# Kernel tuning notes

Hardware: AMD Instinct MI355X
Metric: run time of the kernel (lower is better)

The kernel has to match this reference:

```python
import jax, jax.numpy as jnp
import numpy as np

L, N, E, D, H = 3, 20000, 320000, 128, 4
EPS = 1.1920929e-07  # torch RMSNorm default eps = finfo(float32).eps
NEG_SLOPE = 0.2      # PyG GATConv leaky_relu negative_slope


def rmsnorm(x, w):
    return x * jax.lax.rsqrt(jnp.mean(x * x, axis=-1, keepdims=True) + EPS) * w


def setup_inputs() -> dict:
    key = jax.random.key(0)
    ks = jax.random.split(key, 13)
    s = 0.02
    x = jax.random.normal(ks[0], (N, D), jnp.float32)
    src = jax.random.randint(ks[1], (E,), 0, N, dtype=jnp.int64)
    dst = jax.random.randint(ks[2], (E,), 0, N, dtype=jnp.int64)
    dst = jnp.where(dst == src, (dst + 1) % N, dst)  # no pre-existing self loops
    edge_index = jnp.stack([src, dst])
    return {
        "x": x,
        "W_gat": jax.random.normal(ks[3], (L, D, H * D), jnp.float32) * s,
        "att_src": jax.random.normal(ks[4], (L, H, D), jnp.float32) * s,
        "att_dst": jax.random.normal(ks[5], (L, H, D), jnp.float32) * s,
        "bias_gat": jax.random.normal(ks[6], (L, D), jnp.float32) * s,
        "W1": jax.random.normal(ks[7], (L, D, D), jnp.float32) * s,
        "b1": jax.random.normal(ks[8], (L, D), jnp.float32) * s,
        "W2": jax.random.normal(ks[9], (L, D, D), jnp.float32) * s,
        "b2": jax.random.normal(ks[10], (L, D), jnp.float32) * s,
        "norm1_w": jnp.ones((L, D), jnp.float32),
        "norm2_w": jnp.ones((L, D), jnp.float32),
        "edge_index": edge_index,
    }


def reference(x, W_gat, att_src, att_dst, bias_gat, W1, b1, W2, b2, norm1_w, norm2_w, edge_index):
    # PyG GATConv adds self loops by default
    loops = jnp.arange(N, dtype=edge_index.dtype)
    src = jnp.concatenate([edge_index[0], loops])  # [E+N]
    dst = jnp.concatenate([edge_index[1], loops])
    for i in range(L):
        # --- GATConv(hidden, hidden, heads=H, concat=False), dropout=0 (eval) ---
        xp = (x @ W_gat[i]).reshape(N, H, D)               # [N,H,D]
        a_s = jnp.einsum('nhd,hd->nh', xp, att_src[i])     # [N,H]
        a_d = jnp.einsum('nhd,hd->nh', xp, att_dst[i])
        e = jax.nn.leaky_relu(a_s[src] + a_d[dst], NEG_SLOPE)  # [E+N,H]
        m = jax.ops.segment_max(e, dst, num_segments=N)
        ex = jnp.exp(e - m[dst])
        denom = jax.ops.segment_sum(ex, dst, num_segments=N)
        alpha = ex / denom[dst]                             # segment softmax over incoming edges
        agg = jax.ops.segment_sum(alpha[:, :, None] * xp[src], dst, num_segments=N)  # [N,H,D]
        x_att = agg.mean(axis=1) + bias_gat[i]              # concat=False -> head mean, then bias
        # --- residual + RMSNorm ---
        x = rmsnorm(x + x_att, norm1_w[i])
        # --- FFN ---
        h = jax.nn.relu(x @ W1[i] + b1[i])
        h = h @ W2[i] + b2[i]
        x = rmsnorm(x + h, norm2_w[i])
    return x
```

## Files before the change

kernel.cpp:

```cpp
#include <hip/hip_runtime.h>
#include <hip/hip_bf16.h>

#define N_NODES 20000
#define NEDGE   320000
#define DIM     128
#define NH      4
#define HD      512
#define LAYERS  3
#define EPS_RMS 1.1920929e-07f
#define SLOPE   0.2f
#define NTILES  (N_NODES >> 4)

typedef __bf16 bf16_t;
typedef __bf16 bf16v2 __attribute__((ext_vector_type(2)));
typedef __bf16 bf16v8 __attribute__((ext_vector_type(8)));
typedef float  f32v4  __attribute__((ext_vector_type(4)));
typedef float  f32v2  __attribute__((ext_vector_type(2)));

__device__ __forceinline__ int clamp_node(int s) {
    return ((unsigned)s >= (unsigned)N_NODES) ? 0 : s;
}
__device__ __forceinline__ float leaky(float e) { return e > 0.f ? e : SLOPE * e; }
__device__ __forceinline__ unsigned char enc_fp8(float v) {
    int p = __builtin_amdgcn_cvt_pk_fp8_f32(v, v, 0, false);
    return (unsigned char)(p & 0xff);
}
__device__ __forceinline__ unsigned short enc_fp8_pair(float a, float b) {
    int p = __builtin_amdgcn_cvt_pk_fp8_f32(a, b, 0, false);
    return (unsigned short)(p & 0xffff);
}

__device__ __forceinline__ bool wave_detect_bf16(const unsigned short* xh) {
    int lane = threadIdx.x & 63;
    unsigned short hw = xh[2 * lane];
    int e = (hw >> 7) & 0xff;
    unsigned long long b = __ballot(e >= 96 && e <= 140);
    return __popcll(b) >= 48;
}
__device__ __forceinline__ bool wave_detect_i64(const int* ei) {
    int lane = threadIdx.x & 63;
    unsigned long long b = __ballot(ei[2 * lane + 1] != 0);
    return b == 0ULL;
}
__device__ __forceinline__ float raw_elem(const void* in, size_t j, bool isbf) {
    return isbf ? (float)((const bf16_t*)in)[j] : ((const float*)in)[j];
}
__device__ __forceinline__ bf16_t cvt_elem(const void* in, size_t j, bool isbf) {
    return isbf ? ((const bf16_t*)in)[j] : (bf16_t)((const float*)in)[j];
}
__device__ __forceinline__ int edge_src(const int* ei, int e, bool is64) {
    return clamp_node(is64 ? ei[2 * e] : ei[e]);
}
__device__ __forceinline__ int edge_dst(const int* ei, int e, bool is64) {
    return clamp_node(is64 ? ei[2 * NEDGE + 2 * e] : ei[NEDGE + e]);
}

__global__ __launch_bounds__(256) void prep_v(const void* x, const void* Wg,
                                              const void* aS, const void* aD,
                                              float* __restrict__ vS, float* __restrict__ vD,
                                              int* __restrict__ deg) {
    int gid = blockIdx.x * 256 + threadIdx.x;
    for (int i = gid; i < N_NODES; i += gridDim.x * 256) deg[i] = 0;
    bool isbf = wave_detect_bf16((const unsigned short*)x);
    int w = gid >> 6;
    if (w >= LAYERS * DIM * NH * 2) return;
    int lane = threadIdx.x & 63;
    int sd = w & 1, h = (w >> 1) & 3, k = (w >> 3) & 127, l = w >> 10;
    const void* att = sd ? aD : aS;
    size_t wbase = (size_t)l * DIM * HD + (size_t)k * HD + h * DIM;
    size_t abase = (size_t)l * NH * DIM + (size_t)h * DIM;
    int c = 2 * lane;
    float p = raw_elem(Wg, wbase + c, isbf) * raw_elem(att, abase + c, isbf)
            + raw_elem(Wg, wbase + c + 1, isbf) * raw_elem(att, abase + c + 1, isbf);
#pragma unroll
    for (int msk = 1; msk < 64; msk <<= 1) p += __shfl_xor(p, msk);
    if (lane == 0) {
        float* dst = sd ? vD : vS;
        dst[l * HD + h * DIM + k] = p;
    }
}

__global__ __launch_bounds__(256) void mega_setup(
        const void* x, const void* Wg, const void* W1, const void* W2,
        const void* bg, const void* b1, const void* b2, const void* n1, const void* n2,
        bf16_t* xb, bf16_t* WmixP, bf16_t* W1P, bf16_t* W2P,
        bf16_t* bgc, bf16_t* b1c, bf16_t* b2c, bf16_t* n1c, bf16_t* n2c,
        const int* ei, int* deg,
        const float* vS, const float* vD,
        float* a_s, float* a_d, unsigned short* x8,
        int convBlocks, int histBlocks) {
    const int NX  = N_NODES * DIM;
    const int NWG = LAYERS * DIM * HD;
    const int NW1 = LAYERS * DIM * DIM;
    const int NV  = LAYERS * DIM;
    int b = (int)blockIdx.x;
    if (b >= convBlocks + histBlocks) {
        bool isbf = wave_detect_bf16((const unsigned short*)x);
        int lane = threadIdx.x & 63;
        int n = (b - convBlocks - histBlocks) * 4 + (int)(threadIdx.x >> 6);
        if (n >= N_NODES) return;
        int c = 2 * lane;
        float f0 = raw_elem(x, (size_t)n * DIM + c, isbf);
        float f1 = raw_elem(x, (size_t)n * DIM + c + 1, isbf);
        x8[n * 64 + lane] = enc_fp8_pair(f0, f1);
#pragma unroll
        for (int h = 0; h < NH; ++h) {
            float ps = f0 * vS[h * DIM + c] + f1 * vS[h * DIM + c + 1];
            float pd = f0 * vD[h * DIM + c] + f1 * vD[h * DIM + c + 1];
#pragma unroll
            for (int msk = 1; msk < 64; msk <<= 1) {
                ps += __shfl_xor(ps, msk);
                pd += __shfl_xor(pd, msk);
            }
            if (lane == 0) {
                a_s[n * 4 + h] = ps;
                a_d[n * 4 + h] = pd;
            }
        }
        return;
    }
    if (b >= convBlocks) {
        bool is64 = wave_detect_i64(ei);
        int e = (b - convBlocks) * 256 + threadIdx.x;
        if (e < NEDGE) atomicAdd(&deg[edge_dst(ei, e, is64)], 1);
        return;
    }
    bool isbf = wave_detect_bf16((const unsigned short*)x);
    int i = b * 256 + threadIdx.x;
    if (i < NX) { xb[i] = cvt_elem(x, i, isbf); return; }
    i -= NX;
    if (i < NWG) {
        int l = i >> 16;
        int r = i & 65535;
        int j = r & 7;
        int lane2 = (r >> 3) & 63;
        int mm = lane2 & 15, kqq = lane2 >> 4;
        int tt = (r >> 9) & 1;
        int kk = (r >> 10) & 15;
        int wvv = r >> 14;
        int kidx = kk * 32 + kqq * 8 + j;
        int h = kidx >> 7, kp = kidx & 127;
        int c = 32 * wvv + tt * 16 + mm;
        WmixP[i] = cvt_elem(Wg, (size_t)l * DIM * HD + (size_t)kp * HD + h * DIM + c, isbf);
        return;
    }
    i -= NWG;
    if (i < NW1) {
        int l = i / 16384;
        int r = i & 16383;
        int j = r & 7;
        int lane2 = (r >> 3) & 63;
        int mm = lane2 & 15, kqq = lane2 >> 4;
        int tt = (r >> 9) & 1;
        int ks = (r >> 10) & 3;
        int wvv = r >> 12;
        int k = ks * 32 + kqq * 8 + j;
        int c = 32 * wvv + tt * 16 + mm;
        W1P[i] = cvt_elem(W1, (size_t)l * DIM * DIM + (size_t)k * DIM + c, isbf);
        return;
    }
    i -= NW1;
    if (i < NW1) {
        int l = i / 16384;
        int r = i & 16383;
        int j = r & 7;
        int lane2 = (r >> 3) & 63;
        int mm = lane2 & 15, kqq = lane2 >> 4;
        int tt = (r >> 9) & 1;
        int ks = (r >> 10) & 3;
        int wvv = r >> 12;
        int k = ks * 32 + kqq * 8 + j;
        int c = 32 * wvv + tt * 16 + mm;
        W2P[i] = cvt_elem(W2, (size_t)l * DIM * DIM + (size_t)k * DIM + c, isbf);
        return;
    }
    i -= NW1;
    if (i >= 5 * NV) return;
    int seg = i / NV, k = i - seg * NV;
    if (seg == 0) bgc[k] = cvt_elem(bg, k, isbf);
    else if (seg == 1) b1c[k] = cvt_elem(b1, k, isbf);
    else if (seg == 2) b2c[k] = cvt_elem(b2, k, isbf);
    else if (seg == 3) n1c[k] = cvt_elem(n1, k, isbf);
    else n2c[k] = cvt_elem(n2, k, isbf);
}

__global__ __launch_bounds__(1024) void scan_kernel(const int* __restrict__ deg,
                                                    int* __restrict__ row_ptr,
                                                    int* __restrict__ cursor) {
    __shared__ int wsum[16];
    int tid = threadIdx.x, lane = tid & 63, wv = tid >> 6;
    int v[20];
    int base = tid * 20;
    int tot = 0;
    if (base < N_NODES) {
        const int4* d4 = reinterpret_cast<const int4*>(deg + base);
#pragma unroll
        for (int j = 0; j < 5; ++j) {
            int4 q = d4[j];
            v[4 * j]     = q.x;
            v[4 * j + 1] = q.y;
            v[4 * j + 2] = q.z;
            v[4 * j + 3] = q.w;
        }
#pragma unroll
        for (int i = 0; i < 20; ++i) tot += v[i];
    }
    int x = tot;
#pragma unroll
    for (int off = 1; off < 64; off <<= 1) {
        int t = __shfl_up(x, off);
        if (lane >= off) x += t;
    }
    if (lane == 63) wsum[wv] = x;
    __syncthreads();
    if (wv == 0) {
        int s = (lane < 16) ? wsum[lane] : 0;
#pragma unroll
        for (int off = 1; off < 16; off <<= 1) {
            int t = __shfl_up(s, off);
            if (lane >= off) s += t;
        }
        if (lane < 16) wsum[lane] = s;
    }
    __syncthreads();
    int off0 = ((wv == 0) ? 0 : wsum[wv - 1]) + (x - tot);
    if (tid == 0) row_ptr[0] = 0;
    if (base < N_NODES) {
        int run = off0;
#pragma unroll
        for (int i = 0; i < 20; ++i) {
            run += v[i];
            row_ptr[base + i + 1] = run;
            cursor[base + i] = run - v[i];
        }
    }
}

__global__ void fill_kernel(const int* __restrict__ ei, int* __restrict__ cursor,
                            int* __restrict__ csr_src) {
    bool is64 = wave_detect_i64(ei);
    int e = blockIdx.x * blockDim.x + threadIdx.x;
    if (e < NEDGE) {
        int d = edge_dst(ei, e, is64);
        int pos = atomicAdd(&cursor[d], 1);
        if ((unsigned)pos < (unsigned)NEDGE) csr_src[pos] = edge_src(ei, e, is64);
    }
}

__global__ __launch_bounds__(256) void gat_gather(const int* __restrict__ row_ptr,
                                                  const int* __restrict__ csr_src,
                                                  const float* __restrict__ a_s,
                                                  const float* __restrict__ a_d,
                                                  const unsigned short* __restrict__ x8,
                                                  bf16_t* __restrict__ y) {
    __shared__ float4 wsh[4][64];
    __shared__ int    ssh[4][64];
    int n = (int)((blockIdx.x * blockDim.x + threadIdx.x) >> 6);
    if (n >= N_NODES) return;
    int wv = (int)(threadIdx.x >> 6) & 3;
    int lane = threadIdx.x & 63;
    int beg = row_ptr[n];
    int deg = row_ptr[n + 1] - beg;
    if (deg < 0) deg = 0;
    if (deg > NEDGE) deg = NEDGE;
    if (beg < 0) beg = 0;
    if (beg > NEDGE - deg) beg = NEDGE - deg;

    const float4* a_s4 = reinterpret_cast<const float4*>(a_s);
    const float4 adv = reinterpret_cast<const float4*>(a_d)[n];
    const float4 avs = a_s4[n];
    unsigned short pself = x8[n * 64 + lane];
    float4 wself = {__expf(leaky(avs.x + adv.x)), __expf(leaky(avs.y + adv.y)),
                    __expf(leaky(avs.z + adv.z)), __expf(leaky(avs.w + adv.w))};

    float acc[8];
    {
        f32v2 f = __builtin_amdgcn_cvt_pk_f32_fp8((int)pself, false);
        acc[0] = wself.x * f[0]; acc[1] = wself.x * f[1];
        acc[2] = wself.y * f[0]; acc[3] = wself.y * f[1];
        acc[4] = wself.z * f[0]; acc[5] = wself.z * f[1];
        acc[6] = wself.w * f[0]; acc[7] = wself.w * f[1];
    }

    float4 zl = {0.f, 0.f, 0.f, 0.f};
    for (int c0 = 0; c0 < deg; c0 += 64) {
        int cnt = deg - c0; if (cnt > 64) cnt = 64;
        if (lane < cnt) {
            int s = clamp_node(csr_src[beg + c0 + lane]);
            float4 av = a_s4[s];
            float4 w = {__expf(leaky(av.x + adv.x)), __expf(leaky(av.y + adv.y)),
                        __expf(leaky(av.z + adv.z)), __expf(leaky(av.w + adv.w))};
            zl.x += w.x; zl.y += w.y; zl.z += w.z; zl.w += w.w;
            wsh[wv][lane] = w;
            ssh[wv][lane] = s << 6;
        }
        for (int u0 = 0; u0 < cnt; u0 += 8) {
            int uc = cnt - u0; if (uc > 8) uc = 8;
            unsigned short xe[8]; float4 w[8];
#pragma unroll
            for (int u = 0; u < 8; ++u) {
                if (u < uc) {
                    int sb = ssh[wv][u0 + u];
                    w[u] = wsh[wv][u0 + u];
                    xe[u] = x8[sb + lane];
                }
            }
#pragma unroll
            for (int u = 0; u < 8; ++u) {
                if (u < uc) {
                    f32v2 f = __builtin_amdgcn_cvt_pk_f32_fp8((int)xe[u], false);
                    acc[0] += w[u].x * f[0]; acc[1] += w[u].x * f[1];
                    acc[2] += w[u].y * f[0]; acc[3] += w[u].y * f[1];
                    acc[4] += w[u].z * f[0]; acc[5] += w[u].z * f[1];
                    acc[6] += w[u].w * f[0]; acc[7] += w[u].w * f[1];
                }
            }
        }
    }
    float4 zr = zl;
#pragma unroll
    for (int msk = 1; msk < 64; msk <<= 1) {
        zr.x += __shfl_xor(zr.x, msk);
        zr.y += __shfl_xor(zr.y, msk);
        zr.z += __shfl_xor(zr.z, msk);
        zr.w += __shfl_xor(zr.w, msk);
    }
    float4 z4 = {wself.x + zr.x, wself.y + zr.y, wself.z + zr.z, wself.w + zr.w};
    float4 ih4 = {1.f / z4.x, 1.f / z4.y, 1.f / z4.z, 1.f / z4.w};
    int c = 2 * lane;
#pragma unroll
    for (int h = 0; h < NH; ++h) {
        float ih = h == 0 ? ih4.x : h == 1 ? ih4.y : h == 2 ? ih4.z : ih4.w;
        bf16v2 o;
        o[0] = (bf16_t)(acc[h * 2 + 0] * ih);
        o[1] = (bf16_t)(acc[h * 2 + 1] * ih);
        *reinterpret_cast<bf16v2*>(&y[(size_t)n * HD + h * DIM + c]) = o;
    }
}

template <int MODE>
__global__ __launch_bounds__(256) void mix_ffn(
        const bf16_t* __restrict__ y,
        const bf16_t* __restrict__ WmixP, const bf16_t* __restrict__ bg,
        const bf16_t* __restrict__ n1w, const bf16_t* __restrict__ xb,
        const bf16_t* __restrict__ W1P, const bf16_t* __restrict__ b1,
        const bf16_t* __restrict__ W2P, const bf16_t* __restrict__ b2,
        const bf16_t* __restrict__ n2w, void* __restrict__ out,
        const float* __restrict__ vS, const float* __restrict__ vD,
        float* __restrict__ a_s_n, float* __restrict__ a_d_n,
        unsigned char* __restrict__ x8_n) {
    __shared__ bf16_t ylds[16][524];
    __shared__ bf16_t xm[16][140];
    __shared__ float  ssq_p[16][4];
    __shared__ float  asd_p[4][16][8];
    bf16_t (*hh)[140] = reinterpret_cast<bf16_t (*)[140]>(&ylds[0][0]);

    int tile = blockIdx.x;
    int wv = threadIdx.x >> 6;
    int lane = threadIdx.x & 63;
    int m = lane & 15, kq = lane >> 4;

    const bf16_t* ybase = y + (size_t)tile * 16 * HD;
#pragma unroll
    for (int it = 0; it < 8; ++it) {
        int f = it * 2048 + (int)threadIdx.x * 8;
        int row = f >> 9, col = f & 511;
        *reinterpret_cast<bf16v8*>(&ylds[row][col]) =
            *reinterpret_cast<const bf16v8*>(ybase + f);
    }
    __syncthreads();

    f32v4 accm[2];
    accm[0] = (f32v4){0.f, 0.f, 0.f, 0.f};
    accm[1] = (f32v4){0.f, 0.f, 0.f, 0.f};
#pragma unroll
    for (int kk = 0; kk < 16; ++kk) {
        bf16v8 a = *reinterpret_cast<const bf16v8*>(&ylds[m][kk * 32 + kq * 8]);
#pragma unroll
        for (int tt = 0; tt < 2; ++tt) {
            bf16v8 b = *reinterpret_cast<const bf16v8*>(
                WmixP + ((((wv * 16 + kk) * 2 + tt) << 9) + lane * 8));
            accm[tt] = __builtin_amdgcn_mfma_f32_16x16x32_bf16(a, b, accm[tt], 0, 0, 0);
        }
    }
    float vals[2][4];
    {
        float sp[4] = {0.f, 0.f, 0.f, 0.f};
#pragma unroll
        for (int tt = 0; tt < 2; ++tt) {
            int col = 32 * wv + tt * 16 + m;
            float bv = (float)bg[col];
#pragma unroll
            for (int r = 0; r < 4; ++r) {
                int gr = tile * 16 + kq * 4 + r;
                float v = 0.25f * accm[tt][r] + bv + (float)xb[(size_t)gr * DIM + col];
                vals[tt][r] = v;
                sp[r] += v * v;
            }
        }
#pragma unroll
        for (int r = 0; r < 4; ++r) {
            sp[r] += __shfl_xor(sp[r], 1); sp[r] += __shfl_xor(sp[r], 2);
            sp[r] += __shfl_xor(sp[r], 4); sp[r] += __shfl_xor(sp[r], 8);
            if (m == r) ssq_p[kq * 4 + r][wv] = sp[r];
        }
    }
    __syncthreads();
    {
#pragma unroll
        for (int r = 0; r < 4; ++r) {
            int row = kq * 4 + r;
            float s = ssq_p[row][0] + ssq_p[row][1] + ssq_p[row][2] + ssq_p[row][3];
            float scale = rsqrtf(s * (1.f / 128.f) + EPS_RMS);
#pragma unroll
            for (int tt = 0; tt < 2; ++tt) {
                int col = 32 * wv + tt * 16 + m;
                xm[row][col] = (bf16_t)(vals[tt][r] * scale * (float)n1w[col]);
            }
        }
    }
    __syncthreads();

    f32v4 acc1[2];
    acc1[0] = (f32v4){0.f, 0.f, 0.f, 0.f};
    acc1[1] = (f32v4){0.f, 0.f, 0.f, 0.f};
#pragma unroll
    for (int ks = 0; ks < 4; ++ks) {
        bf16v8 a = *reinterpret_cast<const bf16v8*>(&xm[m][ks * 32 + kq * 8]);
#pragma unroll
        for (int tt = 0; tt < 2; ++tt) {
            bf16v8 b = *reinterpret_cast<const bf16v8*>(
                W1P + ((((wv * 4 + ks) * 2 + tt) << 9) + lane * 8));
            acc1[tt] = __builtin_amdgcn_mfma_f32_16x16x32_bf16(a, b, acc1[tt], 0, 0, 0);
        }
    }
#pragma unroll
    for (int tt = 0; tt < 2; ++tt) {
        int col = 32 * wv + tt * 16 + m;
        float bv = (float)b1[col];
#pragma unroll
        for (int r = 0; r < 4; ++r) {
            float v = acc1[tt][r] + bv;
            hh[kq * 4 + r][col] = (bf16_t)(v > 0.f ? v : 0.f);
        }
    }
    __syncthreads();
    f32v4 acc2[2];
    acc2[0] = (f32v4){0.f, 0.f, 0.f, 0.f};
    acc2[1] = (f32v4){0.f, 0.f, 0.f, 0.f};
#pragma unroll
    for (int ks = 0; ks < 4; ++ks) {
        bf16v8 a = *reinterpret_cast<const bf16v8*>(&hh[m][ks * 32 + kq * 8]);
#pragma unroll
        for (int tt = 0; tt < 2; ++tt) {
            bf16v8 b = *reinterpret_cast<const bf16v8*>(
                W2P + ((((wv * 4 + ks) * 2 + tt) << 9) + lane * 8));
            acc2[tt] = __builtin_amdgcn_mfma_f32_16x16x32_bf16(a, b, acc2[tt], 0, 0, 0);
        }
    }
    float vals2[2][4];
    {
        float sp[4] = {0.f, 0.f, 0.f, 0.f};
#pragma unroll
        for (int tt = 0; tt < 2; ++tt) {
            int col = 32 * wv + tt * 16 + m;
            float bv = (float)b2[col];
#pragma unroll
            for (int r = 0; r < 4; ++r) {
                float v = acc2[tt][r] + bv + (float)xm[kq * 4 + r][col];
                vals2[tt][r] = v;
                sp[r] += v * v;
            }
        }
#pragma unroll
        for (int r = 0; r < 4; ++r) {
            sp[r] += __shfl_xor(sp[r], 1); sp[r] += __shfl_xor(sp[r], 2);
            sp[r] += __shfl_xor(sp[r], 4); sp[r] += __shfl_xor(sp[r], 8);
            if (m == r) ssq_p[kq * 4 + r][wv] = sp[r];
        }
    }
    __syncthreads();
    float o2[2][4];
#pragma unroll
    for (int r = 0; r < 4; ++r) {
        int row = kq * 4 + r;
        int gr = tile * 16 + row;
        float s = ssq_p[row][0] + ssq_p[row][1] + ssq_p[row][2] + ssq_p[row][3];
        float scale = rsqrtf(s * (1.f / 128.f) + EPS_RMS);
#pragma unroll
        for (int tt = 0; tt < 2; ++tt) {
            int col = 32 * wv + tt * 16 + m;
            float o = vals2[tt][r] * scale * (float)n2w[col];
            o2[tt][r] = o;
            if (MODE == 1) ((float*)out)[(size_t)gr * DIM + col] = o;
            else {
                ((bf16_t*)out)[(size_t)gr * DIM + col] = (bf16_t)o;
                x8_n[(size_t)gr * DIM + col] = enc_fp8(o);
            }
        }
    }
    if (MODE == 0) {
        float vs0[NH], vs1[NH], vd0[NH], vd1[NH];
        int col0 = 32 * wv + m, col1 = col0 + 16;
#pragma unroll
        for (int h = 0; h < NH; ++h) {
            vs0[h] = vS[h * DIM + col0]; vs1[h] = vS[h * DIM + col1];
            vd0[h] = vD[h * DIM + col0]; vd1[h] = vD[h * DIM + col1];
        }
#pragma unroll
        for (int r = 0; r < 4; ++r) {
#pragma unroll
            for (int h = 0; h < NH; ++h) {
                float ps = o2[0][r] * vs0[h] + o2[1][r] * vs1[h];
                float pd = o2[0][r] * vd0[h] + o2[1][r] * vd1[h];
                ps += __shfl_xor(ps, 1); ps += __shfl_xor(ps, 2);
                ps += __shfl_xor(ps, 4); ps += __shfl_xor(ps, 8);
                pd += __shfl_xor(pd, 1); pd += __shfl_xor(pd, 2);
                pd += __shfl_xor(pd, 4); pd += __shfl_xor(pd, 8);
                if (m == r * 4 + h) {
                    asd_p[wv][kq * 4 + r][h * 2 + 0] = ps;
                    asd_p[wv][kq * 4 + r][h * 2 + 1] = pd;
                }
            }
        }
        __syncthreads();
        int t = threadIdx.x;
        if (t < 128) {
            int row = t >> 3, idx = t & 7;
            float s = asd_p[0][row][idx] + asd_p[1][row][idx]
                    + asd_p[2][row][idx] + asd_p[3][row][idx];
            int gr = tile * 16 + row;
            if (idx & 1) a_d_n[gr * 4 + (idx >> 1)] = s;
            else         a_s_n[gr * 4 + (idx >> 1)] = s;
        }
    }
}

extern "C" void kernel_launch(void* const* d_in, const int* in_sizes, int n_in,
                              void* d_out, int out_size, void* d_ws, size_t ws_size,
                              hipStream_t stream) {
    const void* x_in   = d_in[0];
    const void* W_gat  = d_in[1];
    const void* att_s  = d_in[2];
    const void* att_d  = d_in[3];
    const void* bias_g = d_in[4];
    const void* W1     = d_in[5];
    const void* b1     = d_in[6];
    const void* W2     = d_in[7];
    const void* b2     = d_in[8];
    const void* n1w    = d_in[9];
    const void* n2w    = d_in[10];
    const int*  ei     = (const int*)d_in[11];

    char* ws = (char*)d_ws;
    size_t off = 0;
    auto alloc = [&](size_t bytes) {
        void* p = ws + off;
        off = (off + bytes + 255) & ~(size_t)255;
        return p;
    };
    bf16_t* WmixP   = (bf16_t*)alloc((size_t)LAYERS * HD * DIM * 2);
    bf16_t* W1P     = (bf16_t*)alloc((size_t)LAYERS * DIM * DIM * 2);
    bf16_t* W2P     = (bf16_t*)alloc((size_t)LAYERS * DIM * DIM * 2);
    bf16_t* xb      = (bf16_t*)alloc((size_t)N_NODES * DIM * 2);
    bf16_t* y       = (bf16_t*)alloc((size_t)N_NODES * HD * 2);
    unsigned short* x8a = (unsigned short*)alloc((size_t)N_NODES * DIM);
    unsigned short* x8b = (unsigned short*)alloc((size_t)N_NODES * DIM);
    float*  vS      = (float*)alloc((size_t)LAYERS * HD * 4);
    float*  vD      = (float*)alloc((size_t)LAYERS * HD * 4);
    float*  a_sA    = (float*)alloc((size_t)N_NODES * NH * 4);
    float*  a_dA    = (float*)alloc((size_t)N_NODES * NH * 4);
    float*  a_sB    = (float*)alloc((size_t)N_NODES * NH * 4);
    float*  a_dB    = (float*)alloc((size_t)N_NODES * NH * 4);
    int*    deg     = (int*)alloc((size_t)N_NODES * 4);
    int*    cursor  = (int*)alloc((size_t)N_NODES * 4);
    int*    row_ptr = (int*)alloc((size_t)(N_NODES + 1) * 4);
    int*    csr     = (int*)alloc((size_t)NEDGE * 4);
    bf16_t* bgc     = (bf16_t*)alloc((size_t)LAYERS * DIM * 2);
    bf16_t* b1c     = (bf16_t*)alloc((size_t)LAYERS * DIM * 2);
    bf16_t* b2c     = (bf16_t*)alloc((size_t)LAYERS * DIM * 2);
    bf16_t* n1c     = (bf16_t*)alloc((size_t)LAYERS * DIM * 2);
    bf16_t* n2c     = (bf16_t*)alloc((size_t)LAYERS * DIM * 2);

    prep_v<<<(LAYERS * DIM * NH * 2 * 64 + 255) / 256, 256, 0, stream>>>(
        x_in, W_gat, att_s, att_d, vS, vD, deg);

    const int NTOT = N_NODES * DIM + LAYERS * DIM * HD + 2 * LAYERS * DIM * DIM
                   + 5 * LAYERS * DIM;
    const int convBlocks = (NTOT + 255) / 256;
    const int histBlocks = (NEDGE + 255) / 256;
    const int asdBlocks  = (N_NODES + 3) / 4;
    mega_setup<<<convBlocks + histBlocks + asdBlocks, 256, 0, stream>>>(
        x_in, W_gat, W1, W2, bias_g, b1, b2, n1w, n2w,
        xb, WmixP, W1P, W2P, bgc, b1c, b2c, n1c, n2c,
        ei, deg, vS, vD, a_sA, a_dA, x8a, convBlocks, histBlocks);

    scan_kernel<<<1, 1024, 0, stream>>>(deg, row_ptr, cursor);
    fill_kernel<<<(NEDGE + 255) / 256, 256, 0, stream>>>(ei, cursor, csr);

    unsigned short* x8cur[2] = {x8a, x8b};
    float* asCur[2] = {a_sA, a_sB};
    float* adCur[2] = {a_dA, a_dB};
    for (int l = 0; l < LAYERS; ++l) {
        int ci = l & 1, ni = (l + 1) & 1;
        gat_gather<<<(N_NODES * 64 + 255) / 256, 256, 0, stream>>>(
            row_ptr, csr, asCur[ci], adCur[ci], x8cur[ci], y);
        if (l < LAYERS - 1) {
            mix_ffn<0><<<NTILES, 256, 0, stream>>>(
                y, WmixP + (size_t)l * HD * DIM, bgc + (size_t)l * DIM,
                n1c + (size_t)l * DIM, xb,
                W1P + (size_t)l * DIM * DIM, b1c + (size_t)l * DIM,
                W2P + (size_t)l * DIM * DIM, b2c + (size_t)l * DIM,
                n2c + (size_t)l * DIM, xb,
                vS + (size_t)(l + 1) * HD, vD + (size_t)(l + 1) * HD,
                asCur[ni], adCur[ni], (unsigned char*)x8cur[ni]);
        } else {
            mix_ffn<1><<<NTILES, 256, 0, stream>>>(
                y, WmixP + (size_t)l * HD * DIM, bgc + (size_t)l * DIM,
                n1c + (size_t)l * DIM, xb,
                W1P + (size_t)l * DIM * DIM, b1c + (size_t)l * DIM,
                W2P + (size_t)l * DIM * DIM, b2c + (size_t)l * DIM,
                n2c + (size_t)l * DIM, d_out,
                nullptr, nullptr, nullptr, nullptr, nullptr);
        }
    }
}
```

Measured before the change: 313.3 us.

## Fuse whole pipeline into one persistent cooperative kernel with grid syncs

Replaces the sequence of setup, scan, fill, gather and mix/FFN launches with a single cooperative persistent kernel. Phases are separated by grid-wide barriers and use grid-stride loops sized from occupancy queries. The aim is to remove launch gaps and tail effects across roughly ten kernels. The cost is grid-sync overhead, a block count capped at 1024, and a single-block scan phase that may serialize. A fallback to the multi-kernel path is kept.

```diff
diff --git a/kernel.cpp b/kernel.cpp
--- a/kernel.cpp
+++ b/kernel.cpp
@@ -1,5 +1,8 @@
 #include <hip/hip_runtime.h>
 #include <hip/hip_bf16.h>
+#include <hip/hip_cooperative_groups.h>
+
+namespace cg = cooperative_groups;
 
 #define N_NODES 20000
 #define NEDGE   320000
@@ -11,6 +14,13 @@
 #define SLOPE   0.2f
 #define NTILES  (N_NODES >> 4)
 
+#define NWGC  (LAYERS * DIM * HD)
+#define NW1C  (LAYERS * DIM * DIM)
+#define NVC   (LAYERS * DIM)
+#define NPACK (NWGC + 2 * NW1C + 5 * NVC)
+
+#define SMEM_BYTES 23552
+
 typedef __bf16 bf16_t;
 typedef __bf16 bf16v2 __attribute__((ext_vector_type(2)));
 typedef __bf16 bf16v8 __attribute__((ext_vector_type(8)));
@@ -54,6 +64,529 @@
 __device__ __forceinline__ int edge_dst(const int* ei, int e, bool is64) {
     return clamp_node(is64 ? ei[2 * NEDGE + 2 * e] : ei[NEDGE + e]);
 }
+
+
+__device__ __forceinline__ void pack_item(int i, bool isbf,
+        const void* Wg, const void* W1, const void* W2,
+        const void* bg, const void* b1, const void* b2,
+        const void* n1, const void* n2,
+        bf16_t* WmixP, bf16_t* W1P, bf16_t* W2P,
+        bf16_t* bgc, bf16_t* b1c, bf16_t* b2c, bf16_t* n1c, bf16_t* n2c) {
+    if (i < NWGC) {
+        int l = i >> 16;
+        int r = i & 65535;
+        int j = r & 7;
+        int lane2 = (r >> 3) & 63;
+        int mm = lane2 & 15, kqq = lane2 >> 4;
+        int tt = (r >> 9) & 1;
+        int kk = (r >> 10) & 15;
+        int wvv = r >> 14;
+        int kidx = kk * 32 + kqq * 8 + j;
+        int h = kidx >> 7, kp = kidx & 127;
+        int c = 32 * wvv + tt * 16 + mm;
+        WmixP[i] = cvt_elem(Wg, (size_t)l * DIM * HD + (size_t)kp * HD + h * DIM + c, isbf);
+        return;
+    }
+    i -= NWGC;
+    if (i < NW1C) {
+        int l = i / 16384;
+        int r = i & 16383;
+        int j = r & 7;
+        int lane2 = (r >> 3) & 63;
+        int mm = lane2 & 15, kqq = lane2 >> 4;
+        int tt = (r >> 9) & 1;
+        int ks = (r >> 10) & 3;
+        int wvv = r >> 12;
+        int k = ks * 32 + kqq * 8 + j;
+        int c = 32 * wvv + tt * 16 + mm;
+        W1P[i] = cvt_elem(W1, (size_t)l * DIM * DIM + (size_t)k * DIM + c, isbf);
+        return;
+    }
+    i -= NW1C;
+    if (i < NW1C) {
+        int l = i / 16384;
+        int r = i & 16383;
+        int j = r & 7;
+        int lane2 = (r >> 3) & 63;
+        int mm = lane2 & 15, kqq = lane2 >> 4;
+        int tt = (r >> 9) & 1;
+        int ks = (r >> 10) & 3;
+        int wvv = r >> 12;
+        int k = ks * 32 + kqq * 8 + j;
+        int c = 32 * wvv + tt * 16 + mm;
+        W2P[i] = cvt_elem(W2, (size_t)l * DIM * DIM + (size_t)k * DIM + c, isbf);
+        return;
+    }
+    i -= NW1C;
+    if (i >= 5 * NVC) return;
+    int seg = i / NVC, k = i - seg * NVC;
+    if (seg == 0) bgc[k] = cvt_elem(bg, k, isbf);
+    else if (seg == 1) b1c[k] = cvt_elem(b1, k, isbf);
+    else if (seg == 2) b2c[k] = cvt_elem(b2, k, isbf);
+    else if (seg == 3) n1c[k] = cvt_elem(n1, k, isbf);
+    else n2c[k] = cvt_elem(n2, k, isbf);
+}
+
+__device__ __forceinline__ void asd_node(int n, int lane, bool isbf, const void* x,
+        const float* __restrict__ vS, const float* __restrict__ vD,
+        float* __restrict__ a_s, float* __restrict__ a_d,
+        unsigned short* __restrict__ x8) {
+    int c = 2 * lane;
+    float f0 = raw_elem(x, (size_t)n * DIM + c, isbf);
+    float f1 = raw_elem(x, (size_t)n * DIM + c + 1, isbf);
+    x8[n * 64 + lane] = enc_fp8_pair(f0, f1);
+#pragma unroll
+    for (int h = 0; h < NH; ++h) {
+        float ps = f0 * vS[h * DIM + c] + f1 * vS[h * DIM + c + 1];
+        float pd = f0 * vD[h * DIM + c] + f1 * vD[h * DIM + c + 1];
+#pragma unroll
+        for (int msk = 1; msk < 64; msk <<= 1) {
+            ps += __shfl_xor(ps, msk);
+            pd += __shfl_xor(pd, msk);
+        }
+        if (lane == 0) {
+            a_s[n * 4 + h] = ps;
+            a_d[n * 4 + h] = pd;
+        }
+    }
+}
+
+__device__ __forceinline__ void gather_node(int n, int lane,
+        float4* wshw, int* sshw,
+        const int* __restrict__ row_ptr, const int* __restrict__ csr_src,
+        const float* __restrict__ a_s, const float* __restrict__ a_d,
+        const unsigned short* __restrict__ x8, bf16_t* __restrict__ y) {
+    int beg = row_ptr[n];
+    int deg = row_ptr[n + 1] - beg;
+    if (deg < 0) deg = 0;
+    if (deg > NEDGE) deg = NEDGE;
+    if (beg < 0) beg = 0;
+    if (beg > NEDGE - deg) beg = NEDGE - deg;
+
+    const float4* a_s4 = reinterpret_cast<const float4*>(a_s);
+    const float4 adv = reinterpret_cast<const float4*>(a_d)[n];
+    const float4 avs = a_s4[n];
+    unsigned short pself = x8[n * 64 + lane];
+    float4 wself = {__expf(leaky(avs.x + adv.x)), __expf(leaky(avs.y + adv.y)),
+                    __expf(leaky(avs.z + adv.z)), __expf(leaky(avs.w + adv.w))};
+
+    float acc[8];
+    {
+        f32v2 f = __builtin_amdgcn_cvt_pk_f32_fp8((int)pself, false);
+        acc[0] = wself.x * f[0]; acc[1] = wself.x * f[1];
+        acc[2] = wself.y * f[0]; acc[3] = wself.y * f[1];
+        acc[4] = wself.z * f[0]; acc[5] = wself.z * f[1];
+        acc[6] = wself.w * f[0]; acc[7] = wself.w * f[1];
+    }
+
+    float4 zl = {0.f, 0.f, 0.f, 0.f};
+    for (int c0 = 0; c0 < deg; c0 += 64) {
+        int cnt = deg - c0; if (cnt > 64) cnt = 64;
+        if (lane < cnt) {
+            int s = clamp_node(csr_src[beg + c0 + lane]);
+            float4 av = a_s4[s];
+            float4 w = {__expf(leaky(av.x + adv.x)), __expf(leaky(av.y + adv.y)),
+                        __expf(leaky(av.z + adv.z)), __expf(leaky(av.w + adv.w))};
+            zl.x += w.x; zl.y += w.y; zl.z += w.z; zl.w += w.w;
+            wshw[lane] = w;
+            sshw[lane] = s << 6;
+        }
+        for (int u0 = 0; u0 < cnt; u0 += 8) {
+            int uc = cnt - u0; if (uc > 8) uc = 8;
+            unsigned short xe[8]; float4 w[8];
+#pragma unroll
+            for (int u = 0; u < 8; ++u) {
+                if (u < uc) {
+                    int sb = sshw[u0 + u];
+                    w[u] = wshw[u0 + u];
+                    xe[u] = x8[sb + lane];
+                }
+            }
+#pragma unroll
+            for (int u = 0; u < 8; ++u) {
+                if (u < uc) {
+                    f32v2 f = __builtin_amdgcn_cvt_pk_f32_fp8((int)xe[u], false);
+                    acc[0] += w[u].x * f[0]; acc[1] += w[u].x * f[1];
+                    acc[2] += w[u].y * f[0]; acc[3] += w[u].y * f[1];
+                    acc[4] += w[u].z * f[0]; acc[5] += w[u].z * f[1];
+                    acc[6] += w[u].w * f[0]; acc[7] += w[u].w * f[1];
+                }
+            }
+        }
+    }
+    float4 zr = zl;
+#pragma unroll
+    for (int msk = 1; msk < 64; msk <<= 1) {
+        zr.x += __shfl_xor(zr.x, msk);
+        zr.y += __shfl_xor(zr.y, msk);
+        zr.z += __shfl_xor(zr.z, msk);
+        zr.w += __shfl_xor(zr.w, msk);
+    }
+    float4 z4 = {wself.x + zr.x, wself.y + zr.y, wself.z + zr.z, wself.w + zr.w};
+    float4 ih4 = {1.f / z4.x, 1.f / z4.y, 1.f / z4.z, 1.f / z4.w};
+    int c = 2 * lane;
+#pragma unroll
+    for (int h = 0; h < NH; ++h) {
+        float ih = h == 0 ? ih4.x : h == 1 ? ih4.y : h == 2 ? ih4.z : ih4.w;
+        bf16v2 o;
+        o[0] = (bf16_t)(acc[h * 2 + 0] * ih);
+        o[1] = (bf16_t)(acc[h * 2 + 1] * ih);
+        *reinterpret_cast<bf16v2*>(&y[(size_t)n * HD + h * DIM + c]) = o;
+    }
+}
+
+__device__ __forceinline__ void mix_tile(char* smem, int tile, bool last,
+        const bf16_t* __restrict__ y,
+        const bf16_t* __restrict__ WmixP, const bf16_t* __restrict__ bg,
+        const bf16_t* __restrict__ n1w, const bf16_t* xb,
+        const bf16_t* __restrict__ W1P, const bf16_t* __restrict__ b1,
+        const bf16_t* __restrict__ W2P, const bf16_t* __restrict__ b2,
+        const bf16_t* __restrict__ n2w, void* out,
+        const float* __restrict__ vS, const float* __restrict__ vD,
+        float* __restrict__ a_s_n, float* __restrict__ a_d_n,
+        unsigned char* __restrict__ x8_n) {
+    bf16_t (*ylds)[524]    = reinterpret_cast<bf16_t(*)[524]>(smem);
+    bf16_t (*xm)[140]      = reinterpret_cast<bf16_t(*)[140]>(smem + 16768);
+    float  (*ssq_p)[4]     = reinterpret_cast<float(*)[4]>(smem + 21248);
+    float  (*asd_p)[16][8] = reinterpret_cast<float(*)[16][8]>(smem + 21504);
+    bf16_t (*hh)[140]      = reinterpret_cast<bf16_t(*)[140]>(smem);
+
+    int wv = (int)threadIdx.x >> 6;
+    int lane = (int)threadIdx.x & 63;
+    int m = lane & 15, kq = lane >> 4;
+
+    const bf16_t* ybase = y + (size_t)tile * 16 * HD;
+#pragma unroll
+    for (int it = 0; it < 8; ++it) {
+        int f = it * 2048 + (int)threadIdx.x * 8;
+        int row = f >> 9, col = f & 511;
+        *reinterpret_cast<bf16v8*>(&ylds[row][col]) =
+            *reinterpret_cast<const bf16v8*>(ybase + f);
+    }
+    __syncthreads();
+
+    f32v4 accm[2];
+    accm[0] = (f32v4){0.f, 0.f, 0.f, 0.f};
+    accm[1] = (f32v4){0.f, 0.f, 0.f, 0.f};
+#pragma unroll
+    for (int kk = 0; kk < 16; ++kk) {
+        bf16v8 a = *reinterpret_cast<const bf16v8*>(&ylds[m][kk * 32 + kq * 8]);
+#pragma unroll
+        for (int tt = 0; tt < 2; ++tt) {
+            bf16v8 b = *reinterpret_cast<const bf16v8*>(
+                WmixP + ((((wv * 16 + kk) * 2 + tt) << 9) + lane * 8));
+            accm[tt] = __builtin_amdgcn_mfma_f32_16x16x32_bf16(a, b, accm[tt], 0, 0, 0);
+        }
+    }
+    float vals[2][4];
+    {
+        float sp[4] = {0.f, 0.f, 0.f, 0.f};
+#pragma unroll
+        for (int tt = 0; tt < 2; ++tt) {
+            int col = 32 * wv + tt * 16 + m;
+            float bv = (float)bg[col];
+#pragma unroll
+            for (int r = 0; r < 4; ++r) {
+                int gr = tile * 16 + kq * 4 + r;
+                float v = 0.25f * accm[tt][r] + bv + (float)xb[(size_t)gr * DIM + col];
+                vals[tt][r] = v;
+                sp[r] += v * v;
+            }
+        }
+#pragma unroll
+        for (int r = 0; r < 4; ++r) {
+            sp[r] += __shfl_xor(sp[r], 1); sp[r] += __shfl_xor(sp[r], 2);
+            sp[r] += __shfl_xor(sp[r], 4); sp[r] += __shfl_xor(sp[r], 8);
+            if (m == r) ssq_p[kq * 4 + r][wv] = sp[r];
+        }
+    }
+    __syncthreads();
+    {
+#pragma unroll
+        for (int r = 0; r < 4; ++r) {
+            int row = kq * 4 + r;
+            float s = ssq_p[row][0] + ssq_p[row][1] + ssq_p[row][2] + ssq_p[row][3];
+            float scale = rsqrtf(s * (1.f / 128.f) + EPS_RMS);
+#pragma unroll
+            for (int tt = 0; tt < 2; ++tt) {
+                int col = 32 * wv + tt * 16 + m;
+                xm[row][col] = (bf16_t)(vals[tt][r] * scale * (float)n1w[col]);
+            }
+        }
+    }
+    __syncthreads();
+
+    f32v4 acc1[2];
+    acc1[0] = (f32v4){0.f, 0.f, 0.f, 0.f};
+    acc1[1] = (f32v4){0.f, 0.f, 0.f, 0.f};
+#pragma unroll
+    for (int ks = 0; ks < 4; ++ks) {
+        bf16v8 a = *reinterpret_cast<const bf16v8*>(&xm[m][ks * 32 + kq * 8]);
+#pragma unroll
+        for (int tt = 0; tt < 2; ++tt) {
+            bf16v8 b = *reinterpret_cast<const bf16v8*>(
+                W1P + ((((wv * 4 + ks) * 2 + tt) << 9) + lane * 8));
+            acc1[tt] = __builtin_amdgcn_mfma_f32_16x16x32_bf16(a, b, acc1[tt], 0, 0, 0);
+        }
+    }
+#pragma unroll
+    for (int tt = 0; tt < 2; ++tt) {
+        int col = 32 * wv + tt * 16 + m;
+        float bv = (float)b1[col];
+#pragma unroll
+        for (int r = 0; r < 4; ++r) {
+            float v = acc1[tt][r] + bv;
+            hh[kq * 4 + r][col] = (bf16_t)(v > 0.f ? v : 0.f);
+        }
+    }
+    __syncthreads();
+    f32v4 acc2[2];
+    acc2[0] = (f32v4){0.f, 0.f, 0.f, 0.f};
+    acc2[1] = (f32v4){0.f, 0.f, 0.f, 0.f};
+#pragma unroll
+    for (int ks = 0; ks < 4; ++ks) {
+        bf16v8 a = *reinterpret_cast<const bf16v8*>(&hh[m][ks * 32 + kq * 8]);
+#pragma unroll
+        for (int tt = 0; tt < 2; ++tt) {
+            bf16v8 b = *reinterpret_cast<const bf16v8*>(
+                W2P + ((((wv * 4 + ks) * 2 + tt) << 9) + lane * 8));
+            acc2[tt] = __builtin_amdgcn_mfma_f32_16x16x32_bf16(a, b, acc2[tt], 0, 0, 0);
+        }
+    }
+    float vals2[2][4];
+    {
+        float sp[4] = {0.f, 0.f, 0.f, 0.f};
+#pragma unroll
+        for (int tt = 0; tt < 2; ++tt) {
+            int col = 32 * wv + tt * 16 + m;
+            float bv = (float)b2[col];
+#pragma unroll
+            for (int r = 0; r < 4; ++r) {
+                float v = acc2[tt][r] + bv + (float)xm[kq * 4 + r][col];
+                vals2[tt][r] = v;
+                sp[r] += v * v;
+            }
+        }
+#pragma unroll
+        for (int r = 0; r < 4; ++r) {
+            sp[r] += __shfl_xor(sp[r], 1); sp[r] += __shfl_xor(sp[r], 2);
+            sp[r] += __shfl_xor(sp[r], 4); sp[r] += __shfl_xor(sp[r], 8);
+            if (m == r) ssq_p[kq * 4 + r][wv] = sp[r];
+        }
+    }
+    __syncthreads();
+    float o2[2][4];
+#pragma unroll
+    for (int r = 0; r < 4; ++r) {
+        int row = kq * 4 + r;
+        int gr = tile * 16 + row;
+        float s = ssq_p[row][0] + ssq_p[row][1] + ssq_p[row][2] + ssq_p[row][3];
+        float scale = rsqrtf(s * (1.f / 128.f) + EPS_RMS);
+#pragma unroll
+        for (int tt = 0; tt < 2; ++tt) {
+            int col = 32 * wv + tt * 16 + m;
+            float o = vals2[tt][r] * scale * (float)n2w[col];
+            o2[tt][r] = o;
+            if (last) ((float*)out)[(size_t)gr * DIM + col] = o;
+            else {
+                ((bf16_t*)out)[(size_t)gr * DIM + col] = (bf16_t)o;
+                x8_n[(size_t)gr * DIM + col] = enc_fp8(o);
+            }
+        }
+    }
+    if (!last) {
+        float vs0[NH], vs1[NH], vd0[NH], vd1[NH];
+        int col0 = 32 * wv + m, col1 = col0 + 16;
+#pragma unroll
+        for (int h = 0; h < NH; ++h) {
+            vs0[h] = vS[h * DIM + col0]; vs1[h] = vS[h * DIM + col1];
+            vd0[h] = vD[h * DIM + col0]; vd1[h] = vD[h * DIM + col1];
+        }
+#pragma unroll
+        for (int r = 0; r < 4; ++r) {
+#pragma unroll
+            for (int h = 0; h < NH; ++h) {
+                float ps = o2[0][r] * vs0[h] + o2[1][r] * vs1[h];
+                float pd = o2[0][r] * vd0[h] + o2[1][r] * vd1[h];
+                ps += __shfl_xor(ps, 1); ps += __shfl_xor(ps, 2);
+                ps += __shfl_xor(ps, 4); ps += __shfl_xor(ps, 8);
+                pd += __shfl_xor(pd, 1); pd += __shfl_xor(pd, 2);
+                pd += __shfl_xor(pd, 4); pd += __shfl_xor(pd, 8);
+                if (m == r * 4 + h) {
+                    asd_p[wv][kq * 4 + r][h * 2 + 0] = ps;
+                    asd_p[wv][kq * 4 + r][h * 2 + 1] = pd;
+                }
+            }
+        }
+        __syncthreads();
+        int t = threadIdx.x;
+        if (t < 128) {
+            int row = t >> 3, idx = t & 7;
+            float s = asd_p[0][row][idx] + asd_p[1][row][idx]
+                    + asd_p[2][row][idx] + asd_p[3][row][idx];
+            int gr = tile * 16 + row;
+            if (idx & 1) a_d_n[gr * 4 + (idx >> 1)] = s;
+            else         a_s_n[gr * 4 + (idx >> 1)] = s;
+        }
+    }
+}
+
+struct Params {
+    const void *x, *Wg, *aS, *aD, *bg, *W1, *b1, *W2, *b2, *n1, *n2;
+    const int* ei;
+    bf16_t *WmixP, *W1P, *W2P, *xb, *y;
+    unsigned short *x8a, *x8b;
+    float *vS, *vD;
+    float *a_sA, *a_dA, *a_sB, *a_dB;
+    int *deg, *cursor, *row_ptr, *csr;
+    bf16_t *bgc, *b1c, *b2c, *n1c, *n2c;
+    void* out;
+};
+
+__global__ __launch_bounds__(256, 4) void fused_all(Params p) {
+    __shared__ __align__(16) char smem[SMEM_BYTES];
+    cg::grid_group grid = cg::this_grid();
+    const int NBLK  = (int)gridDim.x;
+    const int NTH   = NBLK * 256;
+    const int NWAVE = NBLK * 4;
+    int b = (int)blockIdx.x, t = (int)threadIdx.x;
+    int wv = t >> 6, lane = t & 63;
+    int gtid = b * 256 + t;
+    int gwave = b * 4 + wv;
+    bool isbf = wave_detect_bf16((const unsigned short*)p.x);
+    bool is64 = wave_detect_i64(p.ei);
+
+    for (int i = gtid; i < N_NODES; i += NTH) p.deg[i] = 0;
+    for (int w = gwave; w < LAYERS * DIM * NH * 2; w += NWAVE) {
+        int sd = w & 1, h = (w >> 1) & 3, k = (w >> 3) & 127, l = w >> 10;
+        const void* att = sd ? p.aD : p.aS;
+        size_t wbase = (size_t)l * DIM * HD + (size_t)k * HD + h * DIM;
+        size_t abase = (size_t)l * NH * DIM + (size_t)h * DIM;
+        int c = 2 * lane;
+        float pr = raw_elem(p.Wg, wbase + c, isbf) * raw_elem(att, abase + c, isbf)
+                 + raw_elem(p.Wg, wbase + c + 1, isbf) * raw_elem(att, abase + c + 1, isbf);
+#pragma unroll
+        for (int msk = 1; msk < 64; msk <<= 1) pr += __shfl_xor(pr, msk);
+        if (lane == 0) (sd ? p.vD : p.vS)[l * HD + h * DIM + k] = pr;
+    }
+    {
+        const int NV8 = N_NODES * DIM / 8;
+        if (isbf) {
+            const bf16v8* src = (const bf16v8*)p.x;
+            bf16v8* dst = (bf16v8*)p.xb;
+            for (int i = gtid; i < NV8; i += NTH) dst[i] = src[i];
+        } else {
+            const float4* src = (const float4*)p.x;
+            bf16v8* dst = (bf16v8*)p.xb;
+            for (int i = gtid; i < NV8; i += NTH) {
+                float4 a = src[2 * i], bq = src[2 * i + 1];
+                bf16v8 o;
+                o[0] = (bf16_t)a.x;  o[1] = (bf16_t)a.y;
+                o[2] = (bf16_t)a.z;  o[3] = (bf16_t)a.w;
+                o[4] = (bf16_t)bq.x; o[5] = (bf16_t)bq.y;
+                o[6] = (bf16_t)bq.z; o[7] = (bf16_t)bq.w;
+                dst[i] = o;
+            }
+        }
+    }
+    grid.sync();
+
+    {
+        int histB = NBLK >> 3;
+        int asdB  = NBLK >> 2;
+        if (b < histB) {
+            for (int e = b * 256 + t; e < NEDGE; e += histB * 256)
+                atomicAdd(&p.deg[edge_dst(p.ei, e, is64)], 1);
+        } else if (b < histB + asdB) {
+            int aw = (b - histB) * 4 + wv;
+            int astr = asdB * 4;
+            for (int n = aw; n < N_NODES; n += astr)
+                asd_node(n, lane, isbf, p.x, p.vS, p.vD, p.a_sA, p.a_dA, p.x8a);
+        } else {
+            int packB = NBLK - histB - asdB;
+            int pstr = packB * 256;
+            for (int i = (b - histB - asdB) * 256 + t; i < NPACK; i += pstr)
+                pack_item(i, isbf, p.Wg, p.W1, p.W2, p.bg, p.b1, p.b2, p.n1, p.n2,
+                          p.WmixP, p.W1P, p.W2P, p.bgc, p.b1c, p.b2c, p.n1c, p.n2c);
+        }
+    }
+    grid.sync();
+
+    if (b == 0) {
+        int* wsum = (int*)smem;
+        int base = t * 80;
+        int tot = 0;
+        if (base < N_NODES) {
+            const int4* d4 = (const int4*)(p.deg + base);
+#pragma unroll
+            for (int j = 0; j < 20; ++j) {
+                int4 q = d4[j];
+                tot += q.x + q.y + q.z + q.w;
+            }
+        }
+        int x = tot;
+#pragma unroll
+        for (int off = 1; off < 64; off <<= 1) {
+            int tv = __shfl_up(x, off);
+            if (lane >= off) x += tv;
+        }
+        if (lane == 63) wsum[wv] = x;
+        __syncthreads();
+        int woff = 0;
+        for (int j = 0; j < wv; ++j) woff += wsum[j];
+        int run = woff + (x - tot);
+        if (t == 0) p.row_ptr[0] = 0;
+        if (base < N_NODES) {
+            const int4* d4 = (const int4*)(p.deg + base);
+#pragma unroll
+            for (int j = 0; j < 20; ++j) {
+                int4 q = d4[j];
+                int n = base + 4 * j;
+                p.cursor[n] = run;     run += q.x; p.row_ptr[n + 1] = run;
+                p.cursor[n + 1] = run; run += q.y; p.row_ptr[n + 2] = run;
+                p.cursor[n + 2] = run; run += q.z; p.row_ptr[n + 3] = run;
+                p.cursor[n + 3] = run; run += q.w; p.row_ptr[n + 4] = run;
+            }
+        }
+    }
+    grid.sync();
+
+    for (int e = gtid; e < NEDGE; e += NTH) {
+        int d = edge_dst(p.ei, e, is64);
+        int pos = atomicAdd(&p.cursor[d], 1);
+        if ((unsigned)pos < (unsigned)NEDGE) p.csr[pos] = edge_src(p.ei, e, is64);
+    }
+    grid.sync();
+
+    unsigned short* x8cur[2] = {p.x8a, p.x8b};
+    float* asCur[2] = {p.a_sA, p.a_sB};
+    float* adCur[2] = {p.a_dA, p.a_dB};
+#pragma unroll
+    for (int l = 0; l < LAYERS; ++l) {
+        int ci = l & 1, ni = (l + 1) & 1;
+        {
+            float4* wshw = (float4*)smem + wv * 64;
+            int* sshw = (int*)(smem + 4096) + wv * 64;
+            for (int n = gwave; n < N_NODES; n += NWAVE)
+                gather_node(n, lane, wshw, sshw, p.row_ptr, p.csr,
+                            asCur[ci], adCur[ci], x8cur[ci], p.y);
+        }
+        grid.sync();
+        bool last = (l == LAYERS - 1);
+        for (int tile = b; tile < NTILES; tile += NBLK) {
+            mix_tile(smem, tile, last,
+                     p.y, p.WmixP + (size_t)l * HD * DIM, p.bgc + l * DIM,
+                     p.n1c + l * DIM, p.xb,
+                     p.W1P + (size_t)l * DIM * DIM, p.b1c + l * DIM,
+                     p.W2P + (size_t)l * DIM * DIM, p.b2c + l * DIM,
+                     p.n2c + l * DIM, last ? p.out : (void*)p.xb,
+                     p.vS + (size_t)(l + 1) * HD, p.vD + (size_t)(l + 1) * HD,
+                     asCur[ni], adCur[ni], (unsigned char*)x8cur[ni]);
+        }
+        if (!last) grid.sync();
+    }
+}
+
 
 __global__ __launch_bounds__(256) void prep_v(const void* x, const void* Wg,
                                               const void* aS, const void* aD,
@@ -89,34 +622,14 @@
         const float* vS, const float* vD,
         float* a_s, float* a_d, unsigned short* x8,
         int convBlocks, int histBlocks) {
-    const int NX  = N_NODES * DIM;
-    const int NWG = LAYERS * DIM * HD;
-    const int NW1 = LAYERS * DIM * DIM;
-    const int NV  = LAYERS * DIM;
+    const int NX = N_NODES * DIM;
     int b = (int)blockIdx.x;
     if (b >= convBlocks + histBlocks) {
         bool isbf = wave_detect_bf16((const unsigned short*)x);
         int lane = threadIdx.x & 63;
         int n = (b - convBlocks - histBlocks) * 4 + (int)(threadIdx.x >> 6);
         if (n >= N_NODES) return;
-        int c = 2 * lane;
-        float f0 = raw_elem(x, (size_t)n * DIM + c, isbf);
-        float f1 = raw_elem(x, (size_t)n * DIM + c + 1, isbf);
-        x8[n * 64 + lane] = enc_fp8_pair(f0, f1);
-#pragma unroll
-        for (int h = 0; h < NH; ++h) {
-            float ps = f0 * vS[h * DIM + c] + f1 * vS[h * DIM + c + 1];
-            float pd = f0 * vD[h * DIM + c] + f1 * vD[h * DIM + c + 1];
-#pragma unroll
-            for (int msk = 1; msk < 64; msk <<= 1) {
-                ps += __shfl_xor(ps, msk);
-                pd += __shfl_xor(pd, msk);
-            }
-            if (lane == 0) {
-                a_s[n * 4 + h] = ps;
-                a_d[n * 4 + h] = pd;
-            }
-        }
+        asd_node(n, lane, isbf, x, vS, vD, a_s, a_d, x8);
         return;
     }
     if (b >= convBlocks) {
@@ -128,60 +641,8 @@
     bool isbf = wave_detect_bf16((const unsigned short*)x);
     int i = b * 256 + threadIdx.x;
     if (i < NX) { xb[i] = cvt_elem(x, i, isbf); return; }
-    i -= NX;
-    if (i < NWG) {
-        int l = i >> 16;
-        int r = i & 65535;
-        int j = r & 7;
-        int lane2 = (r >> 3) & 63;
-        int mm = lane2 & 15, kqq = lane2 >> 4;
-        int tt = (r >> 9) & 1;
-        int kk = (r >> 10) & 15;
-        int wvv = r >> 14;
-        int kidx = kk * 32 + kqq * 8 + j;
-        int h = kidx >> 7, kp = kidx & 127;
-        int c = 32 * wvv + tt * 16 + mm;
-        WmixP[i] = cvt_elem(Wg, (size_t)l * DIM * HD + (size_t)kp * HD + h * DIM + c, isbf);
-        return;
-    }
-    i -= NWG;
-    if (i < NW1) {
-        int l = i / 16384;
-        int r = i & 16383;
-        int j = r & 7;
-        int lane2 = (r >> 3) & 63;
-        int mm = lane2 & 15, kqq = lane2 >> 4;
-        int tt = (r >> 9) & 1;
-        int ks = (r >> 10) & 3;
-        int wvv = r >> 12;
-        int k = ks * 32 + kqq * 8 + j;
-        int c = 32 * wvv + tt * 16 + mm;
-        W1P[i] = cvt_elem(W1, (size_t)l * DIM * DIM + (size_t)k * DIM + c, isbf);
-        return;
-    }
-    i -= NW1;
-    if (i < NW1) {
-        int l = i / 16384;
-        int r = i & 16383;
-        int j = r & 7;
-        int lane2 = (r >> 3) & 63;
-        int mm = lane2 & 15, kqq = lane2 >> 4;
-        int tt = (r >> 9) & 1;
-        int ks = (r >> 10) & 3;
-        int wvv = r >> 12;
-        int k = ks * 32 + kqq * 8 + j;
-        int c = 32 * wvv + tt * 16 + mm;
-        W2P[i] = cvt_elem(W2, (size_t)l * DIM * DIM + (size_t)k * DIM + c, isbf);
-        return;
-    }
-    i -= NW1;
-    if (i >= 5 * NV) return;
-    int seg = i / NV, k = i - seg * NV;
-    if (seg == 0) bgc[k] = cvt_elem(bg, k, isbf);
-    else if (seg == 1) b1c[k] = cvt_elem(b1, k, isbf);
-    else if (seg == 2) b2c[k] = cvt_elem(b2, k, isbf);
-    else if (seg == 3) n1c[k] = cvt_elem(n1, k, isbf);
-    else n2c[k] = cvt_elem(n2, k, isbf);
+    pack_item(i - NX, isbf, Wg, W1, W2, bg, b1, b2, n1, n2,
+              WmixP, W1P, W2P, bgc, b1c, b2c, n1c, n2c);
 }
 
 __global__ __launch_bounds__(1024) void scan_kernel(const int* __restrict__ deg,
@@ -259,281 +720,23 @@
     if (n >= N_NODES) return;
     int wv = (int)(threadIdx.x >> 6) & 3;
     int lane = threadIdx.x & 63;
-    int beg = row_ptr[n];
-    int deg = row_ptr[n + 1] - beg;
-    if (deg < 0) deg = 0;
-    if (deg > NEDGE) deg = NEDGE;
-    if (beg < 0) beg = 0;
-    if (beg > NEDGE - deg) beg = NEDGE - deg;
-
-    const float4* a_s4 = reinterpret_cast<const float4*>(a_s);
-    const float4 adv = reinterpret_cast<const float4*>(a_d)[n];
-    const float4 avs = a_s4[n];
-    unsigned short pself = x8[n * 64 + lane];
-    float4 wself = {__expf(leaky(avs.x + adv.x)), __expf(leaky(avs.y + adv.y)),
-                    __expf(leaky(avs.z + adv.z)), __expf(leaky(avs.w + adv.w))};
-
-    float acc[8];
-    {
-        f32v2 f = __builtin_amdgcn_cvt_pk_f32_fp8((int)pself, false);
-        acc[0] = wself.x * f[0]; acc[1] = wself.x * f[1];
-        acc[2] = wself.y * f[0]; acc[3] = wself.y * f[1];
-        acc[4] = wself.z * f[0]; acc[5] = wself.z * f[1];
-        acc[6] = wself.w * f[0]; acc[7] = wself.w * f[1];
-    }
-
-    float4 zl = {0.f, 0.f, 0.f, 0.f};
-    for (int c0 = 0; c0 < deg; c0 += 64) {
-        int cnt = deg - c0; if (cnt > 64) cnt = 64;
-        if (lane < cnt) {
-            int s = clamp_node(csr_src[beg + c0 + lane]);
-            float4 av = a_s4[s];
-            float4 w = {__expf(leaky(av.x + adv.x)), __expf(leaky(av.y + adv.y)),
-                        __expf(leaky(av.z + adv.z)), __expf(leaky(av.w + adv.w))};
-            zl.x += w.x; zl.y += w.y; zl.z += w.z; zl.w += w.w;
-            wsh[wv][lane] = w;
-            ssh[wv][lane] = s << 6;
-        }
-        for (int u0 = 0; u0 < cnt; u0 += 8) {
-            int uc = cnt - u0; if (uc > 8) uc = 8;
-            unsigned short xe[8]; float4 w[8];
-#pragma unroll
-            for (int u = 0; u < 8; ++u) {
-                if (u < uc) {
-                    int sb = ssh[wv][u0 + u];
-                    w[u] = wsh[wv][u0 + u];
-                    xe[u] = x8[sb + lane];
-                }
-            }
-#pragma unroll
-            for (int u = 0; u < 8; ++u) {
-                if (u < uc) {
-                    f32v2 f = __builtin_amdgcn_cvt_pk_f32_fp8((int)xe[u], false);
-                    acc[0] += w[u].x * f[0]; acc[1] += w[u].x * f[1];
-                    acc[2] += w[u].y * f[0]; acc[3] += w[u].y * f[1];
-                    acc[4] += w[u].z * f[0]; acc[5] += w[u].z * f[1];
-                    acc[6] += w[u].w * f[0]; acc[7] += w[u].w * f[1];
-                }
-            }
-        }
-    }
-    float4 zr = zl;
-#pragma unroll
-    for (int msk = 1; msk < 64; msk <<= 1) {
-        zr.x += __shfl_xor(zr.x, msk);
-        zr.y += __shfl_xor(zr.y, msk);
-        zr.z += __shfl_xor(zr.z, msk);
-        zr.w += __shfl_xor(zr.w, msk);
-    }
-    float4 z4 = {wself.x + zr.x, wself.y + zr.y, wself.z + zr.z, wself.w + zr.w};
-    float4 ih4 = {1.f / z4.x, 1.f / z4.y, 1.f / z4.z, 1.f / z4.w};
-    int c = 2 * lane;
-#pragma unroll
-    for (int h = 0; h < NH; ++h) {
-        float ih = h == 0 ? ih4.x : h == 1 ? ih4.y : h == 2 ? ih4.z : ih4.w;
-        bf16v2 o;
-        o[0] = (bf16_t)(acc[h * 2 + 0] * ih);
-        o[1] = (bf16_t)(acc[h * 2 + 1] * ih);
-        *reinterpret_cast<bf16v2*>(&y[(size_t)n * HD + h * DIM + c]) = o;
-    }
+    gather_node(n, lane, wsh[wv], ssh[wv], row_ptr, csr_src, a_s, a_d, x8, y);
 }
 
 template <int MODE>
 __global__ __launch_bounds__(256) void mix_ffn(
         const bf16_t* __restrict__ y,
         const bf16_t* __restrict__ WmixP, const bf16_t* __restrict__ bg,
-        const bf16_t* __restrict__ n1w, const bf16_t* __restrict__ xb,
+        const bf16_t* __restrict__ n1w, const bf16_t* xb,
         const bf16_t* __restrict__ W1P, const bf16_t* __restrict__ b1,
         const bf16_t* __restrict__ W2P, const bf16_t* __restrict__ b2,
-        const bf16_t* __restrict__ n2w, void* __restrict__ out,
+        const bf16_t* __restrict__ n2w, void* out,
         const float* __restrict__ vS, const float* __restrict__ vD,
         float* __restrict__ a_s_n, float* __restrict__ a_d_n,
         unsigned char* __restrict__ x8_n) {
-    __shared__ bf16_t ylds[16][524];
-    __shared__ bf16_t xm[16][140];
-    __shared__ float  ssq_p[16][4];
-    __shared__ float  asd_p[4][16][8];
-    bf16_t (*hh)[140] = reinterpret_cast<bf16_t (*)[140]>(&ylds[0][0]);
-
-    int tile = blockIdx.x;
-    int wv = threadIdx.x >> 6;
-    int lane = threadIdx.x & 63;
-    int m = lane & 15, kq = lane >> 4;
-
-    const bf16_t* ybase = y + (size_t)tile * 16 * HD;
-#pragma unroll
-    for (int it = 0; it < 8; ++it) {
-        int f = it * 2048 + (int)threadIdx.x * 8;
-        int row = f >> 9, col = f & 511;
-        *reinterpret_cast<bf16v8*>(&ylds[row][col]) =
-            *reinterpret_cast<const bf16v8*>(ybase + f);
-    }
-    __syncthreads();
-
-    f32v4 accm[2];
-    accm[0] = (f32v4){0.f, 0.f, 0.f, 0.f};
-    accm[1] = (f32v4){0.f, 0.f, 0.f, 0.f};
-#pragma unroll
-    for (int kk = 0; kk < 16; ++kk) {
-        bf16v8 a = *reinterpret_cast<const bf16v8*>(&ylds[m][kk * 32 + kq * 8]);
-#pragma unroll
-        for (int tt = 0; tt < 2; ++tt) {
-            bf16v8 b = *reinterpret_cast<const bf16v8*>(
-                WmixP + ((((wv * 16 + kk) * 2 + tt) << 9) + lane * 8));
-            accm[tt] = __builtin_amdgcn_mfma_f32_16x16x32_bf16(a, b, accm[tt], 0, 0, 0);
-        }
-    }
-    float vals[2][4];
-    {
-        float sp[4] = {0.f, 0.f, 0.f, 0.f};
-#pragma unroll
-        for (int tt = 0; tt < 2; ++tt) {
-            int col = 32 * wv + tt * 16 + m;
-            float bv = (float)bg[col];
-#pragma unroll
-            for (int r = 0; r < 4; ++r) {
-                int gr = tile * 16 + kq * 4 + r;
-                float v = 0.25f * accm[tt][r] + bv + (float)xb[(size_t)gr * DIM + col];
-                vals[tt][r] = v;
-                sp[r] += v * v;
-            }
-        }
-#pragma unroll
-        for (int r = 0; r < 4; ++r) {
-            sp[r] += __shfl_xor(sp[r], 1); sp[r] += __shfl_xor(sp[r], 2);
-            sp[r] += __shfl_xor(sp[r], 4); sp[r] += __shfl_xor(sp[r], 8);
-            if (m == r) ssq_p[kq * 4 + r][wv] = sp[r];
-        }
-    }
-    __syncthreads();
-    {
-#pragma unroll
-        for (int r = 0; r < 4; ++r) {
-            int row = kq * 4 + r;
-            float s = ssq_p[row][0] + ssq_p[row][1] + ssq_p[row][2] + ssq_p[row][3];
-            float scale = rsqrtf(s * (1.f / 128.f) + EPS_RMS);
-#pragma unroll
-            for (int tt = 0; tt < 2; ++tt) {
-                int col = 32 * wv + tt * 16 + m;
-                xm[row][col] = (bf16_t)(vals[tt][r] * scale * (float)n1w[col]);
-            }
-        }
-    }
-    __syncthreads();
-
-    f32v4 acc1[2];
-    acc1[0] = (f32v4){0.f, 0.f, 0.f, 0.f};
-    acc1[1] = (f32v4){0.f, 0.f, 0.f, 0.f};
-#pragma unroll
-    for (int ks = 0; ks < 4; ++ks) {
-        bf16v8 a = *reinterpret_cast<const bf16v8*>(&xm[m][ks * 32 + kq * 8]);
-#pragma unroll
-        for (int tt = 0; tt < 2; ++tt) {
-            bf16v8 b = *reinterpret_cast<const bf16v8*>(
-                W1P + ((((wv * 4 + ks) * 2 + tt) << 9) + lane * 8));
-            acc1[tt] = __builtin_amdgcn_mfma_f32_16x16x32_bf16(a, b, acc1[tt], 0, 0, 0);
-        }
-    }
-#pragma unroll
-    for (int tt = 0; tt < 2; ++tt) {
-        int col = 32 * wv + tt * 16 + m;
-        float bv = (float)b1[col];
-#pragma unroll
-        for (int r = 0; r < 4; ++r) {
-            float v = acc1[tt][r] + bv;
-            hh[kq * 4 + r][col] = (bf16_t)(v > 0.f ? v : 0.f);
-        }
-    }
-    __syncthreads();
-    f32v4 acc2[2];
-    acc2[0] = (f32v4){0.f, 0.f, 0.f, 0.f};
-    acc2[1] = (f32v4){0.f, 0.f, 0.f, 0.f};
-#pragma unroll
-    for (int ks = 0; ks < 4; ++ks) {
-        bf16v8 a = *reinterpret_cast<const bf16v8*>(&hh[m][ks * 32 + kq * 8]);
-#pragma unroll
-        for (int tt = 0; tt < 2; ++tt) {
-            bf16v8 b = *reinterpret_cast<const bf16v8*>(
-                W2P + ((((wv * 4 + ks) * 2 + tt) << 9) + lane * 8));
-            acc2[tt] = __builtin_amdgcn_mfma_f32_16x16x32_bf16(a, b, acc2[tt], 0, 0, 0);
-        }
-    }
-    float vals2[2][4];
-    {
-        float sp[4] = {0.f, 0.f, 0.f, 0.f};
-#pragma unroll
-        for (int tt = 0; tt < 2; ++tt) {
-            int col = 32 * wv + tt * 16 + m;
-            float bv = (float)b2[col];
-#pragma unroll
-            for (int r = 0; r < 4; ++r) {
-                float v = acc2[tt][r] + bv + (float)xm[kq * 4 + r][col];
-                vals2[tt][r] = v;
-                sp[r] += v * v;
-            }
-        }
-#pragma unroll
-        for (int r = 0; r < 4; ++r) {
-            sp[r] += __shfl_xor(sp[r], 1); sp[r] += __shfl_xor(sp[r], 2);
-            sp[r] += __shfl_xor(sp[r], 4); sp[r] += __shfl_xor(sp[r], 8);
-            if (m == r) ssq_p[kq * 4 + r][wv] = sp[r];
-        }
-    }
-    __syncthreads();
-    float o2[2][4];
-#pragma unroll
-    for (int r = 0; r < 4; ++r) {
-        int row = kq * 4 + r;
-        int gr = tile * 16 + row;
-        float s = ssq_p[row][0] + ssq_p[row][1] + ssq_p[row][2] + ssq_p[row][3];
-        float scale = rsqrtf(s * (1.f / 128.f) + EPS_RMS);
-#pragma unroll
-        for (int tt = 0; tt < 2; ++tt) {
-            int col = 32 * wv + tt * 16 + m;
-            float o = vals2[tt][r] * scale * (float)n2w[col];
-            o2[tt][r] = o;
-            if (MODE == 1) ((float*)out)[(size_t)gr * DIM + col] = o;
-            else {
-                ((bf16_t*)out)[(size_t)gr * DIM + col] = (bf16_t)o;
-                x8_n[(size_t)gr * DIM + col] = enc_fp8(o);
-            }
-        }
-    }
-    if (MODE == 0) {
-        float vs0[NH], vs1[NH], vd0[NH], vd1[NH];
-        int col0 = 32 * wv + m, col1 = col0 + 16;
-#pragma unroll
-        for (int h = 0; h < NH; ++h) {
-            vs0[h] = vS[h * DIM + col0]; vs1[h] = vS[h * DIM + col1];
-            vd0[h] = vD[h * DIM + col0]; vd1[h] = vD[h * DIM + col1];
-        }
-#pragma unroll
-        for (int r = 0; r < 4; ++r) {
-#pragma unroll
-            for (int h = 0; h < NH; ++h) {
-                float ps = o2[0][r] * vs0[h] + o2[1][r] * vs1[h];
-                float pd = o2[0][r] * vd0[h] + o2[1][r] * vd1[h];
-                ps += __shfl_xor(ps, 1); ps += __shfl_xor(ps, 2);
-                ps += __shfl_xor(ps, 4); ps += __shfl_xor(ps, 8);
-                pd += __shfl_xor(pd, 1); pd += __shfl_xor(pd, 2);
-                pd += __shfl_xor(pd, 4); pd += __shfl_xor(pd, 8);
-                if (m == r * 4 + h) {
-                    asd_p[wv][kq * 4 + r][h * 2 + 0] = ps;
-                    asd_p[wv][kq * 4 + r][h * 2 + 1] = pd;
-                }
-            }
-        }
-        __syncthreads();
-        int t = threadIdx.x;
-        if (t < 128) {
-            int row = t >> 3, idx = t & 7;
-            float s = asd_p[0][row][idx] + asd_p[1][row][idx]
-                    + asd_p[2][row][idx] + asd_p[3][row][idx];
-            int gr = tile * 16 + row;
-            if (idx & 1) a_d_n[gr * 4 + (idx >> 1)] = s;
-            else         a_s_n[gr * 4 + (idx >> 1)] = s;
-        }
-    }
+    __shared__ __align__(16) char smem[SMEM_BYTES];
+    mix_tile(smem, (int)blockIdx.x, MODE == 1, y, WmixP, bg, n1w, xb,
+             W1P, b1, W2P, b2, n2w, out, vS, vD, a_s_n, a_d_n, x8_n);
 }
 
 extern "C" void kernel_launch(void* const* d_in, const int* in_sizes, int n_in,
@@ -582,46 +785,83 @@
     bf16_t* n1c     = (bf16_t*)alloc((size_t)LAYERS * DIM * 2);
     bf16_t* n2c     = (bf16_t*)alloc((size_t)LAYERS * DIM * 2);
 
-    prep_v<<<(LAYERS * DIM * NH * 2 * 64 + 255) / 256, 256, 0, stream>>>(
-        x_in, W_gat, att_s, att_d, vS, vD, deg);
-
-    const int NTOT = N_NODES * DIM + LAYERS * DIM * HD + 2 * LAYERS * DIM * DIM
-                   + 5 * LAYERS * DIM;
-    const int convBlocks = (NTOT + 255) / 256;
-    const int histBlocks = (NEDGE + 255) / 256;
-    const int asdBlocks  = (N_NODES + 3) / 4;
-    mega_setup<<<convBlocks + histBlocks + asdBlocks, 256, 0, stream>>>(
-        x_in, W_gat, W1, W2, bias_g, b1, b2, n1w, n2w,
-        xb, WmixP, W1P, W2P, bgc, b1c, b2c, n1c, n2c,
-        ei, deg, vS, vD, a_sA, a_dA, x8a, convBlocks, histBlocks);
-
-    scan_kernel<<<1, 1024, 0, stream>>>(deg, row_ptr, cursor);
-    fill_kernel<<<(NEDGE + 255) / 256, 256, 0, stream>>>(ei, cursor, csr);
-
-    unsigned short* x8cur[2] = {x8a, x8b};
-    float* asCur[2] = {a_sA, a_sB};
-    float* adCur[2] = {a_dA, a_dB};
-    for (int l = 0; l < LAYERS; ++l) {
-        int ci = l & 1, ni = (l + 1) & 1;
-        gat_gather<<<(N_NODES * 64 + 255) / 256, 256, 0, stream>>>(
-            row_ptr, csr, asCur[ci], adCur[ci], x8cur[ci], y);
-        if (l < LAYERS - 1) {
-            mix_ffn<0><<<NTILES, 256, 0, stream>>>(
-                y, WmixP + (size_t)l * HD * DIM, bgc + (size_t)l * DIM,
-                n1c + (size_t)l * DIM, xb,
-                W1P + (size_t)l * DIM * DIM, b1c + (size_t)l * DIM,
-                W2P + (size_t)l * DIM * DIM, b2c + (size_t)l * DIM,
-                n2c + (size_t)l * DIM, xb,
-                vS + (size_t)(l + 1) * HD, vD + (size_t)(l + 1) * HD,
-                asCur[ni], adCur[ni], (unsigned char*)x8cur[ni]);
-        } else {
-            mix_ffn<1><<<NTILES, 256, 0, stream>>>(
-                y, WmixP + (size_t)l * HD * DIM, bgc + (size_t)l * DIM,
-                n1c + (size_t)l * DIM, xb,
-                W1P + (size_t)l * DIM * DIM, b1c + (size_t)l * DIM,
-                W2P + (size_t)l * DIM * DIM, b2c + (size_t)l * DIM,
-                n2c + (size_t)l * DIM, d_out,
-                nullptr, nullptr, nullptr, nullptr, nullptr);
-        }
-    }
-}
+    static int coopBlocks = -1;
+    if (coopBlocks == -1) {
+        int perCU = 0;
+        int nCU = 256;
+        hipDeviceProp_t prop;
+        int dev = 0;
+        if (hipGetDevice(&dev) == hipSuccess &&
+            hipGetDeviceProperties(&prop, dev) == hipSuccess)
+            nCU = prop.multiProcessorCount;
+        if (hipOccupancyMaxActiveBlocksPerMultiprocessor(
+                &perCU, reinterpret_cast<const void*>(fused_all), 256, 0) != hipSuccess)
+            perCU = 0;
+        long cap = (long)perCU * nCU;
+        coopBlocks = (cap >= 8) ? (int)(cap < 1024 ? cap : 1024) : 0;
+    }
+
+    bool done = false;
+    if (coopBlocks >= 8) {
+        Params prm;
+        prm.x = x_in; prm.Wg = W_gat; prm.aS = att_s; prm.aD = att_d;
+        prm.bg = bias_g; prm.W1 = W1; prm.b1 = b1; prm.W2 = W2; prm.b2 = b2;
+        prm.n1 = n1w; prm.n2 = n2w; prm.ei = ei;
+        prm.WmixP = WmixP; prm.W1P = W1P; prm.W2P = W2P; prm.xb = xb; prm.y = y;
+        prm.x8a = x8a; prm.x8b = x8b; prm.vS = vS; prm.vD = vD;
+        prm.a_sA = a_sA; prm.a_dA = a_dA; prm.a_sB = a_sB; prm.a_dB = a_dB;
+        prm.deg = deg; prm.cursor = cursor; prm.row_ptr = row_ptr; prm.csr = csr;
+        prm.bgc = bgc; prm.b1c = b1c; prm.b2c = b2c; prm.n1c = n1c; prm.n2c = n2c;
+        prm.out = d_out;
+        void* kargs[] = {(void*)&prm};
+        hipError_t err = hipLaunchCooperativeKernel(
+            reinterpret_cast<const void*>(fused_all),
+            dim3(coopBlocks), dim3(256), kargs, 0, stream);
+        if (err == hipSuccess) done = true;
+        else { (void)hipGetLastError(); coopBlocks = 0; }
+    }
+
+    if (!done) {
+        prep_v<<<(LAYERS * DIM * NH * 2 * 64 + 255) / 256, 256, 0, stream>>>(
+            x_in, W_gat, att_s, att_d, vS, vD, deg);
+
+        const int NTOT = N_NODES * DIM + NPACK;
+        const int convBlocks = (NTOT + 255) / 256;
+        const int histBlocks = (NEDGE + 255) / 256;
+        const int asdBlocks  = (N_NODES + 3) / 4;
+        mega_setup<<<convBlocks + histBlocks + asdBlocks, 256, 0, stream>>>(
+            x_in, W_gat, W1, W2, bias_g, b1, b2, n1w, n2w,
+            xb, WmixP, W1P, W2P, bgc, b1c, b2c, n1c, n2c,
+            ei, deg, vS, vD, a_sA, a_dA, x8a, convBlocks, histBlocks);
+
+        scan_kernel<<<1, 1024, 0, stream>>>(deg, row_ptr, cursor);
+        fill_kernel<<<(NEDGE + 255) / 256, 256, 0, stream>>>(ei, cursor, csr);
+
+        unsigned short* x8cur[2] = {x8a, x8b};
+        float* asCur[2] = {a_sA, a_sB};
+        float* adCur[2] = {a_dA, a_dB};
+        for (int l = 0; l < LAYERS; ++l) {
+            int ci = l & 1, ni = (l + 1) & 1;
+            gat_gather<<<(N_NODES * 64 + 255) / 256, 256, 0, stream>>>(
+                row_ptr, csr, asCur[ci], adCur[ci], x8cur[ci], y);
+            if (l < LAYERS - 1) {
+                mix_ffn<0><<<NTILES, 256, 0, stream>>>(
+                    y, WmixP + (size_t)l * HD * DIM, bgc + (size_t)l * DIM,
+                    n1c + (size_t)l * DIM, xb,
+                    W1P + (size_t)l * DIM * DIM, b1c + (size_t)l * DIM,
+                    W2P + (size_t)l * DIM * DIM, b2c + (size_t)l * DIM,
+                    n2c + (size_t)l * DIM, xb,
+                    vS + (size_t)(l + 1) * HD, vD + (size_t)(l + 1) * HD,
+                    asCur[ni], adCur[ni], (unsigned char*)x8cur[ni]);
+            } else {
+                mix_ffn<1><<<NTILES, 256, 0, stream>>>(
+                    y, WmixP + (size_t)l * HD * DIM, bgc + (size_t)l * DIM,
+                    n1c + (size_t)l * DIM, xb,
+                    W1P + (size_t)l * DIM * DIM, b1c + (size_t)l * DIM,
+                    W2P + (size_t)l * DIM * DIM, b2c + (size_t)l * DIM,
+                    n2c + (size_t)l * DIM, d_out,
+                    nullptr, nullptr, nullptr, nullptr, nullptr);
+            }
+        }
+    }
+}
```

New measurement: 1.045 ms. +233.5%, slower.
